# Kernel tuning notes

Measured on AMD Instinct MI355X. Metric: run time of the kernel, lower is better.

The kernel has to match this reference:

```python
import jax, jax.numpy as jnp
import numpy as np

N_NODES = 10000


def _gcn_norm(edge_index, edge_weight, n):
    # PyG GCNConv default: add self-loops (weight 1), symmetric normalization.
    ar = jnp.arange(n, dtype=edge_index.dtype)
    ei = jnp.concatenate([edge_index, jnp.stack([ar, ar])], axis=1)
    ew = jnp.concatenate([edge_weight, jnp.ones((n,), edge_weight.dtype)], axis=0)
    row, col = ei[0], ei[1]
    deg = jax.ops.segment_sum(ew, col, num_segments=n)
    dis = jnp.where(deg > 0, jax.lax.rsqrt(jnp.where(deg > 0, deg, 1.0)), 0.0)
    norm = dis[row] * ew * dis[col]
    return row, col, norm


def _gcn_conv(h, W, b, row, col, norm, n):
    hw = h @ W                                    # [N, out]
    msg = norm[:, None] * hw[row]                 # gather + edge scale
    return jax.ops.segment_sum(msg, col, num_segments=n) + b


def setup_inputs() -> dict:
    key = jax.random.key(0)
    ks = jax.random.split(key, 8)
    N, E, D, H1, H2 = N_NODES, 160000, 256, 128, 64
    return {
        "x": jax.random.normal(ks[0], (N, D), jnp.float32),
        "edge_index": jax.random.randint(ks[1], (2, E), 0, N, jnp.int64 if jax.config.jax_enable_x64 else jnp.int32),
        "edge_weight": jax.random.uniform(ks[2], (E,), jnp.float32),
        "noise": jax.random.normal(ks[3], (N, H2), jnp.float32),
        "W1": jax.random.normal(ks[4], (D, H1), jnp.float32) * (1.0 / np.sqrt(D)),
        "b1": jnp.zeros((H1,), jnp.float32),
        "W2": jax.random.normal(ks[5], (H1, H2), jnp.float32) * (1.0 / np.sqrt(H1)),
        "b2": jnp.zeros((H2,), jnp.float32),
        "W3": jax.random.normal(ks[6], (H1, H2), jnp.float32) * (1.0 / np.sqrt(H1)),
        "b3": jnp.zeros((H2,), jnp.float32),
    }


def reference(x, edge_index, edge_weight, noise, W1, b1, W2, b2, W3, b3):
    n = x.shape[0]
    row, col, norm = _gcn_norm(edge_index, edge_weight, n)
    h = jax.nn.relu(_gcn_conv(x, W1, b1, row, col, norm, n))
    mean = _gcn_conv(h, W2, b2, row, col, norm, n)
    log_std = _gcn_conv(h, W3, b3, row, col, norm, n)
    z = mean + noise * jnp.exp(log_std)           # reparameterization
    adj_rec = jax.nn.sigmoid(z @ z.T)             # [N, N] dot-product decode
    return adj_rec
```

## Files before the change

### kernel.cpp

```cpp
#include <hip/hip_runtime.h>


#define Nn 10000
#define Np 10112
#define NpK (Np * 64)

typedef short short8 __attribute__((ext_vector_type(8)));
typedef float f32x4 __attribute__((ext_vector_type(4)));
typedef unsigned short ushort4e __attribute__((ext_vector_type(4)));

static __device__ __forceinline__ float sigmoidf(float v) {
  return __builtin_amdgcn_rcpf(1.0f + __expf(-v));
}
static __device__ __forceinline__ unsigned short f32_to_bf16(float f) {
  unsigned int u = __float_as_uint(f);
  unsigned int r = (u + 0x7FFF + ((u >> 16) & 1)) >> 16;
  return (unsigned short)r;
}
static __device__ __forceinline__ float bf16_to_f32(unsigned short s) {
  return __uint_as_float(((unsigned int)s) << 16);
}

__global__ void k_init(float* __restrict__ deg, int* __restrict__ cnt, int n,
                       unsigned short* __restrict__ zh, unsigned short* __restrict__ zl) {
  int i = blockIdx.x * 256 + threadIdx.x;
  if (i < n) { deg[i] = 1.0f; cnt[i] = 0; }
  if (i < (Np - Nn) * 64) { zh[Nn * 64 + i] = 0; zl[Nn * 64 + i] = 0; }
}

__global__ void k_edge_pre(const int* __restrict__ col, const float* __restrict__ ew,
                           float* __restrict__ deg, int* __restrict__ cnt, int E) {
  int e = blockIdx.x * 256 + threadIdx.x;
  if (e < E) { int c = col[e]; atomicAdd(&deg[c], ew[e]); atomicAdd(&cnt[c], 1); }
}

__global__ void k_dis(float* __restrict__ deg, int n) {
  int i = blockIdx.x * 256 + threadIdx.x;
  if (i < n) { float d = deg[i]; deg[i] = (d > 0.0f) ? rsqrtf(d) : 0.0f; }
}

__global__ __launch_bounds__(256) void k_scan(const int* __restrict__ cnt,
                                              int* __restrict__ ofs, int* __restrict__ ofs2,
                                              int n) {
  __shared__ int partial[256];
  const int t = threadIdx.x;
  const int CH = (n + 255) / 256;
  const int start = t * CH;
  int local = 0;
  for (int j = 0; j < CH; ++j) {
    int idx = start + j;
    if (idx < n) local += cnt[idx];
  }
  partial[t] = local;
  __syncthreads();
  for (int off = 1; off < 256; off <<= 1) {
    int x = (t >= off) ? partial[t - off] : 0;
    __syncthreads();
    partial[t] += x;
    __syncthreads();
  }
  int run = partial[t] - local;
  for (int j = 0; j < CH; ++j) {
    int idx = start + j;
    if (idx < n) {
      ofs[idx] = run; ofs2[idx] = run;
      run += cnt[idx];
    }
  }
  if (t == 255) { ofs[n] = run; ofs2[n] = run; }
}

__global__ void k_fill(const int* __restrict__ row, const int* __restrict__ col,
                       const float* __restrict__ ew, const float* __restrict__ dis,
                       int* __restrict__ ofs2, int* __restrict__ csr_src,
                       float* __restrict__ csr_w, int E) {
  int e = blockIdx.x * 256 + threadIdx.x;
  if (e < E) {
    int r = row[e], c = col[e];
    int p = atomicAdd(&ofs2[c], 1);
    csr_src[p] = r;
    csr_w[p] = dis[r] * ew[e] * dis[c];
  }
}

__global__ __launch_bounds__(256) void k_gemm1(const float* __restrict__ x,
                                               const float* __restrict__ W1,
                                               float* __restrict__ hw1) {
  __shared__ float xs[16][68];
  __shared__ float ws[64][128];
  const int tid = threadIdx.x;
  const int row0 = blockIdx.x * 16;
  const int j0 = (tid & 31) * 4;
  const int r0 = (tid >> 5) * 2;
  const int lr = tid >> 4, lk = tid & 15;
  float acc0[4] = {0, 0, 0, 0}, acc1[4] = {0, 0, 0, 0};
  for (int k0 = 0; k0 < 256; k0 += 64) {
    *(float4*)&xs[lr][lk * 4] = *(const float4*)&x[(row0 + lr) * 256 + k0 + lk * 4];
#pragma unroll
    for (int it = 0; it < 8; ++it) {
      int idx4 = tid + it * 256;
      int kk = idx4 >> 5, jq = idx4 & 31;
      *(float4*)&ws[kk][jq * 4] = *(const float4*)&W1[(k0 + kk) * 128 + jq * 4];
    }
    __syncthreads();
#pragma unroll 8
    for (int kk = 0; kk < 64; ++kk) {
      float a0 = xs[r0][kk], a1 = xs[r0 + 1][kk];
      float4 w = *(const float4*)&ws[kk][j0];
      acc0[0] += a0 * w.x; acc0[1] += a0 * w.y; acc0[2] += a0 * w.z; acc0[3] += a0 * w.w;
      acc1[0] += a1 * w.x; acc1[1] += a1 * w.y; acc1[2] += a1 * w.z; acc1[3] += a1 * w.w;
    }
    __syncthreads();
  }
  *(float4*)&hw1[(row0 + r0) * 128 + j0] = make_float4(acc0[0], acc0[1], acc0[2], acc0[3]);
  *(float4*)&hw1[(row0 + r0 + 1) * 128 + j0] = make_float4(acc1[0], acc1[1], acc1[2], acc1[3]);
}

__global__ __launch_bounds__(256) void k_agg(const int* __restrict__ ofs,
                                             const int* __restrict__ csr_src,
                                             const float* __restrict__ csr_w,
                                             const float* __restrict__ feat,
                                             const float* __restrict__ dis,
                                             const float* __restrict__ b,
                                             float* __restrict__ out, int n, int mode) {
  int node = blockIdx.x * 4 + (threadIdx.x >> 6);
  if (node >= n) return;
  int f2 = threadIdx.x & 63;
  const float2* featv = (const float2*)feat;
  int s = ofs[node], e = ofs[node + 1];
  float d = dis[node];
  float2 self = featv[node * 64 + f2];
  float accx = d * d * self.x, accy = d * d * self.y;
  int j = s;
  for (; j + 2 <= e; j += 2) {
    int r0 = csr_src[j], r1 = csr_src[j + 1];
    float w0 = csr_w[j], w1 = csr_w[j + 1];
    float2 v0 = featv[r0 * 64 + f2];
    float2 v1 = featv[r1 * 64 + f2];
    accx += w0 * v0.x + w1 * v1.x;
    accy += w0 * v0.y + w1 * v1.y;
  }
  if (j < e) {
    int r0 = csr_src[j];
    float w0 = csr_w[j];
    float2 v0 = featv[r0 * 64 + f2];
    accx += w0 * v0.x;
    accy += w0 * v0.y;
  }
  float2 o;
  if (mode == 0) {
    float2 bb = ((const float2*)b)[f2];
    o.x = fmaxf(accx + bb.x, 0.0f);
    o.y = fmaxf(accy + bb.y, 0.0f);
  } else {
    o.x = accx; o.y = accy;
  }
  ((float2*)out)[node * 64 + f2] = o;
}

__global__ __launch_bounds__(256) void k_gemm2z(const float* __restrict__ hagg,
                                                const float* __restrict__ W2, const float* __restrict__ W3,
                                                const float* __restrict__ b2, const float* __restrict__ b3,
                                                const float* __restrict__ noise,
                                                unsigned short* __restrict__ zh,
                                                unsigned short* __restrict__ zl) {
  __shared__ float xs[16][68];
  __shared__ float ws[64][128];
  __shared__ float zs[16][128];
  const int tid = threadIdx.x;
  const int row0 = blockIdx.x * 16;
  const int j0 = (tid & 31) * 4;
  const int r0 = (tid >> 5) * 2;
  const int lr = tid >> 4, lk = tid & 15;
  float acc0[4] = {0, 0, 0, 0}, acc1[4] = {0, 0, 0, 0};
  for (int k0 = 0; k0 < 128; k0 += 64) {
    *(float4*)&xs[lr][lk * 4] = *(const float4*)&hagg[(row0 + lr) * 128 + k0 + lk * 4];
#pragma unroll
    for (int it = 0; it < 8; ++it) {
      int idx4 = tid + it * 256;
      int kk = idx4 >> 5, jq = idx4 & 31;
      int j = jq * 4;
      float4 wv;
      if (j < 64) wv = *(const float4*)&W2[(k0 + kk) * 64 + j];
      else        wv = *(const float4*)&W3[(k0 + kk) * 64 + (j - 64)];
      *(float4*)&ws[kk][j] = wv;
    }
    __syncthreads();
#pragma unroll 8
    for (int kk = 0; kk < 64; ++kk) {
      float a0 = xs[r0][kk], a1 = xs[r0 + 1][kk];
      float4 w = *(const float4*)&ws[kk][j0];
      acc0[0] += a0 * w.x; acc0[1] += a0 * w.y; acc0[2] += a0 * w.z; acc0[3] += a0 * w.w;
      acc1[0] += a1 * w.x; acc1[1] += a1 * w.y; acc1[2] += a1 * w.z; acc1[3] += a1 * w.w;
    }
    __syncthreads();
  }
  {
    float4 bb = (j0 < 64) ? *(const float4*)&b2[j0] : *(const float4*)&b3[j0 - 64];
    zs[r0][j0 + 0] = acc0[0] + bb.x; zs[r0][j0 + 1] = acc0[1] + bb.y;
    zs[r0][j0 + 2] = acc0[2] + bb.z; zs[r0][j0 + 3] = acc0[3] + bb.w;
    zs[r0 + 1][j0 + 0] = acc1[0] + bb.x; zs[r0 + 1][j0 + 1] = acc1[1] + bb.y;
    zs[r0 + 1][j0 + 2] = acc1[2] + bb.z; zs[r0 + 1][j0 + 3] = acc1[3] + bb.w;
  }
  __syncthreads();
  {
    const int r = tid >> 4;
    const int jj = (tid & 15) * 4;
    float4 mn = *(const float4*)&zs[r][jj];
    float4 ls = *(const float4*)&zs[r][64 + jj];
    float4 nz = *(const float4*)&noise[(row0 + r) * 64 + jj];
    float z0 = mn.x + nz.x * __expf(ls.x);
    float z1 = mn.y + nz.y * __expf(ls.y);
    float z2 = mn.z + nz.z * __expf(ls.z);
    float z3 = mn.w + nz.w * __expf(ls.w);
    ushort4e h, l;
    h[0] = f32_to_bf16(z0); l[0] = f32_to_bf16(z0 - bf16_to_f32(h[0]));
    h[1] = f32_to_bf16(z1); l[1] = f32_to_bf16(z1 - bf16_to_f32(h[1]));
    h[2] = f32_to_bf16(z2); l[2] = f32_to_bf16(z2 - bf16_to_f32(h[2]));
    h[3] = f32_to_bf16(z3); l[3] = f32_to_bf16(z3 - bf16_to_f32(h[3]));
    *(ushort4e*)&zh[(row0 + r) * 64 + jj] = h;
    *(ushort4e*)&zl[(row0 + r) * 64 + jj] = l;
  }
}

__global__ __launch_bounds__(256) void k_decode(const unsigned short* __restrict__ zh,
                                                const unsigned short* __restrict__ zl,
                                                float* __restrict__ out, int n) {
  __shared__ short zhr[128][64];
  __shared__ short zlr[128][64];
  __shared__ short zhc[128][64];
  __shared__ short zlc[128][64];
  const int tid = threadIdx.x;
  const int R0 = blockIdx.y * 128;
  const int C0 = blockIdx.x * 128;

  {
    const int seg = tid & 7;
#pragma unroll
    for (int p = 0; p < 4; ++p) {
      const int rr = (p << 5) + (tid >> 3);
      const int sw = (seg ^ (rr & 7)) * 8;
      short8 vhr = *(const short8*)&zh[(size_t)(R0 + rr) * 64 + seg * 8];
      short8 vlr = *(const short8*)&zl[(size_t)(R0 + rr) * 64 + seg * 8];
      short8 vhc = *(const short8*)&zh[(size_t)(C0 + rr) * 64 + seg * 8];
      short8 vlc = *(const short8*)&zl[(size_t)(C0 + rr) * 64 + seg * 8];
      *(short8*)&zhr[rr][sw] = vhr;
      *(short8*)&zlr[rr][sw] = vlr;
      *(short8*)&zhc[rr][sw] = vhc;
      *(short8*)&zlc[rr][sw] = vlc;
    }
  }
  __syncthreads();

  const int wave = tid >> 6, lane = tid & 63;
  const int lr0 = (wave >> 1) * 64;
  const int lc0 = (wave & 1) * 64;
  const int lrow = lane & 15;
  const int quad = lane >> 4;
  f32x4 acc[4][4];
#pragma unroll
  for (int m = 0; m < 4; ++m)
#pragma unroll
    for (int nn = 0; nn < 4; ++nn) acc[m][nn] = (f32x4){0.0f, 0.0f, 0.0f, 0.0f};

#pragma unroll
  for (int kc = 0; kc < 64; kc += 32) {
    const int cb = (kc >> 3) + quad;
    short8 rh[4], rl[4], ch[4], cl[4];
#pragma unroll
    for (int m = 0; m < 4; ++m) {
      int row = lr0 + m * 16 + lrow;
      int sw = (cb ^ (row & 7)) * 8;
      rh[m] = *(const short8*)&zhr[row][sw];
      rl[m] = *(const short8*)&zlr[row][sw];
    }
#pragma unroll
    for (int nn = 0; nn < 4; ++nn) {
      int row = lc0 + nn * 16 + lrow;
      int sw = (cb ^ (row & 7)) * 8;
      ch[nn] = *(const short8*)&zhc[row][sw];
      cl[nn] = *(const short8*)&zlc[row][sw];
    }
#pragma unroll
    for (int m = 0; m < 4; ++m)
#pragma unroll
      for (int nn = 0; nn < 4; ++nn) {
        acc[m][nn] = __builtin_amdgcn_mfma_f32_16x16x32_bf16(ch[nn], rh[m], acc[m][nn], 0, 0, 0);
        acc[m][nn] = __builtin_amdgcn_mfma_f32_16x16x32_bf16(cl[nn], rh[m], acc[m][nn], 0, 0, 0);
        acc[m][nn] = __builtin_amdgcn_mfma_f32_16x16x32_bf16(ch[nn], rl[m], acc[m][nn], 0, 0, 0);
      }
  }

#pragma unroll
  for (int m = 0; m < 4; ++m) {
    int gr = R0 + lr0 + m * 16 + lrow;
    if (gr >= n) continue;
#pragma unroll
    for (int nn = 0; nn < 4; ++nn) {
      int c0 = C0 + lc0 + nn * 16 + quad * 4;
      if (c0 >= n) continue;
      f32x4 v;
      v[0] = sigmoidf(acc[m][nn][0]);
      v[1] = sigmoidf(acc[m][nn][1]);
      v[2] = sigmoidf(acc[m][nn][2]);
      v[3] = sigmoidf(acc[m][nn][3]);
      *(f32x4*)&out[(size_t)gr * n + c0] = v;
    }
  }
}

extern "C" void kernel_launch(void* const* d_in, const int* in_sizes, int n_in,
                              void* d_out, int out_size, void* d_ws, size_t ws_size,
                              hipStream_t stream) {
  const float* x     = (const float*)d_in[0];
  const int*   ei    = (const int*)d_in[1];
  const float* ew    = (const float*)d_in[2];
  const float* noise = (const float*)d_in[3];
  const float* W1    = (const float*)d_in[4];
  const float* b1    = (const float*)d_in[5];
  const float* W2    = (const float*)d_in[6];
  const float* b2    = (const float*)d_in[7];
  const float* W3    = (const float*)d_in[8];
  const float* b3    = (const float*)d_in[9];
  const int E = in_sizes[2];
  const int n = Nn;
  const int* row = ei;
  const int* col = ei + E;

  float* dis = (float*)d_ws;
  unsigned short* zh = (unsigned short*)((char*)d_ws + 10240 * 4);
  unsigned short* zl = zh + NpK;

  float* S    = (float*)d_out;
  float* hw1  = S;
  float* h    = S + 1310720;
  float* hagg = S + 2621440;
  float* csr_w  = S + 5242880;
  int* csr_src  = (int*)(S + 5402880);
  int* ofs      = (int*)(S + 5562880);
  int* ofs2     = (int*)(S + 5572896);
  int* cnt      = (int*)(S + 5582912);

  k_init<<<(n + 255) / 256, 256, 0, stream>>>(dis, cnt, n, zh, zl);
  k_edge_pre<<<(E + 255) / 256, 256, 0, stream>>>(col, ew, dis, cnt, E);
  k_dis<<<(n + 255) / 256, 256, 0, stream>>>(dis, n);
  k_scan<<<1, 256, 0, stream>>>(cnt, ofs, ofs2, n);
  k_fill<<<(E + 255) / 256, 256, 0, stream>>>(row, col, ew, dis, ofs2, csr_src, csr_w, E);

  k_gemm1<<<n / 16, 256, 0, stream>>>(x, W1, hw1);
  k_agg<<<(n + 3) / 4, 256, 0, stream>>>(ofs, csr_src, csr_w, hw1, dis, b1, h, n, 0);
  k_agg<<<(n + 3) / 4, 256, 0, stream>>>(ofs, csr_src, csr_w, h, dis, b1, hagg, n, 1);

  k_gemm2z<<<n / 16, 256, 0, stream>>>(hagg, W2, W3, b2, b3, noise, zh, zl);

  dim3 g((n + 127) / 128, (n + 127) / 128);
  k_decode<<<g, 256, 0, stream>>>(zh, zl, (float*)d_out, n);
}
```

Measured before the change: 575.4 us.

## Fuse all GCN-VAE stages into one persistent kernel with grid barriers

```diff
diff --git a/kernel.cpp b/kernel.cpp
--- a/kernel.cpp
+++ b/kernel.cpp
@@ -4,10 +4,19 @@
 #define Nn 10000
 #define Np 10112
 #define NpK (Np * 64)
+#define NBLK 448
+#define NTHR (NBLK * 256)
+#define NTILE (79 * 79)
 
 typedef short short8 __attribute__((ext_vector_type(8)));
 typedef float f32x4 __attribute__((ext_vector_type(4)));
 typedef unsigned short ushort4e __attribute__((ext_vector_type(4)));
+
+union SmemT {
+  struct { short zhr[128][64]; short zlr[128][64]; short zhc[128][64]; short zlc[128][64]; } d;
+  struct { float xs[16][68]; float ws[64][128]; float zs[16][128]; } g;
+  int partial[256];
+};
 
 static __device__ __forceinline__ float sigmoidf(float v) {
   return __builtin_amdgcn_rcpf(1.0f + __expf(-v));
@@ -21,290 +30,317 @@
   return __uint_as_float(((unsigned int)s) << 16);
 }
 
-__global__ void k_init(float* __restrict__ deg, int* __restrict__ cnt, int n,
-                       unsigned short* __restrict__ zh, unsigned short* __restrict__ zl) {
-  int i = blockIdx.x * 256 + threadIdx.x;
-  if (i < n) { deg[i] = 1.0f; cnt[i] = 0; }
-  if (i < (Np - Nn) * 64) { zh[Nn * 64 + i] = 0; zl[Nn * 64 + i] = 0; }
-}
-
-__global__ void k_edge_pre(const int* __restrict__ col, const float* __restrict__ ew,
-                           float* __restrict__ deg, int* __restrict__ cnt, int E) {
-  int e = blockIdx.x * 256 + threadIdx.x;
-  if (e < E) { int c = col[e]; atomicAdd(&deg[c], ew[e]); atomicAdd(&cnt[c], 1); }
-}
-
-__global__ void k_dis(float* __restrict__ deg, int n) {
-  int i = blockIdx.x * 256 + threadIdx.x;
-  if (i < n) { float d = deg[i]; deg[i] = (d > 0.0f) ? rsqrtf(d) : 0.0f; }
-}
-
-__global__ __launch_bounds__(256) void k_scan(const int* __restrict__ cnt,
-                                              int* __restrict__ ofs, int* __restrict__ ofs2,
-                                              int n) {
-  __shared__ int partial[256];
-  const int t = threadIdx.x;
-  const int CH = (n + 255) / 256;
-  const int start = t * CH;
-  int local = 0;
-  for (int j = 0; j < CH; ++j) {
-    int idx = start + j;
-    if (idx < n) local += cnt[idx];
-  }
-  partial[t] = local;
+static __device__ __forceinline__ void gsync(unsigned* bar, int slot) {
   __syncthreads();
-  for (int off = 1; off < 256; off <<= 1) {
-    int x = (t >= off) ? partial[t - off] : 0;
-    __syncthreads();
-    partial[t] += x;
-    __syncthreads();
-  }
-  int run = partial[t] - local;
-  for (int j = 0; j < CH; ++j) {
-    int idx = start + j;
-    if (idx < n) {
-      ofs[idx] = run; ofs2[idx] = run;
-      run += cnt[idx];
-    }
-  }
-  if (t == 255) { ofs[n] = run; ofs2[n] = run; }
-}
-
-__global__ void k_fill(const int* __restrict__ row, const int* __restrict__ col,
-                       const float* __restrict__ ew, const float* __restrict__ dis,
-                       int* __restrict__ ofs2, int* __restrict__ csr_src,
-                       float* __restrict__ csr_w, int E) {
-  int e = blockIdx.x * 256 + threadIdx.x;
-  if (e < E) {
-    int r = row[e], c = col[e];
+  if (threadIdx.x == 0) {
+    __hip_atomic_fetch_add(&bar[slot], 1u, __ATOMIC_RELEASE, __HIP_MEMORY_SCOPE_AGENT);
+    while (__hip_atomic_load(&bar[slot], __ATOMIC_RELAXED, __HIP_MEMORY_SCOPE_AGENT) < (unsigned)NBLK)
+      __builtin_amdgcn_s_sleep(2);
+    __threadfence();
+  }
+  __syncthreads();
+}
+
+__global__ void k_barzero(unsigned* __restrict__ bar) {
+  if (threadIdx.x < 16) bar[threadIdx.x] = 0;
+}
+
+__global__ __launch_bounds__(256, 2) void k_mega(
+    const float* __restrict__ x, const int* __restrict__ erow, const int* __restrict__ ecol,
+    const float* __restrict__ ew, const float* __restrict__ noise,
+    const float* __restrict__ W1, const float* __restrict__ b1,
+    const float* __restrict__ W2, const float* __restrict__ b2,
+    const float* __restrict__ W3, const float* __restrict__ b3,
+    float* __restrict__ out, float* __restrict__ dis,
+    unsigned short* __restrict__ zh, unsigned short* __restrict__ zl,
+    unsigned* __restrict__ bar, int E) {
+  __shared__ SmemT sm;
+  const int tid = threadIdx.x;
+  const int bid = blockIdx.x;
+  const int gid = bid * 256 + tid;
+
+  float* S = out;
+  float* hw1  = S;
+  float* h    = S + 1310720;
+  float* hagg = S + 2621440;
+  float* csr_w = S + 5242880;
+  int* csr_src = (int*)(S + 5402880);
+  int* ofs     = (int*)(S + 5562880);
+  int* ofs2    = (int*)(S + 5572896);
+  int* cnt     = (int*)(S + 5582912);
+
+  if (gid < Nn) { dis[gid] = 1.0f; cnt[gid] = 0; }
+  if (gid < (Np - Nn) * 64) { zh[Nn * 64 + gid] = 0; zl[Nn * 64 + gid] = 0; }
+  gsync(bar, 0);
+
+  for (int e = gid; e < E; e += NTHR) {
+    int c = ecol[e];
+    atomicAdd(&dis[c], ew[e]);
+    atomicAdd(&cnt[c], 1);
+  }
+  gsync(bar, 1);
+
+  if (bid == 0) {
+    const int CH = (Nn + 255) / 256;
+    const int start = tid * CH;
+    int local = 0;
+    for (int j = 0; j < CH; ++j) {
+      int idx = start + j;
+      if (idx < Nn) local += cnt[idx];
+    }
+    sm.partial[tid] = local;
+    __syncthreads();
+    for (int off = 1; off < 256; off <<= 1) {
+      int v = (tid >= off) ? sm.partial[tid - off] : 0;
+      __syncthreads();
+      sm.partial[tid] += v;
+      __syncthreads();
+    }
+    int run = sm.partial[tid] - local;
+    for (int j = 0; j < CH; ++j) {
+      int idx = start + j;
+      if (idx < Nn) { ofs[idx] = run; ofs2[idx] = run; run += cnt[idx]; }
+    }
+    if (tid == 255) { ofs[Nn] = run; ofs2[Nn] = run; }
+  } else {
+    int i = (bid - 1) * 256 + tid;
+    if (i < Nn) { float dv = dis[i]; dis[i] = (dv > 0.0f) ? rsqrtf(dv) : 0.0f; }
+  }
+  gsync(bar, 2);
+
+  for (int e = gid; e < E; e += NTHR) {
+    int r = erow[e], c = ecol[e];
     int p = atomicAdd(&ofs2[c], 1);
     csr_src[p] = r;
     csr_w[p] = dis[r] * ew[e] * dis[c];
   }
-}
-
-__global__ __launch_bounds__(256) void k_gemm1(const float* __restrict__ x,
-                                               const float* __restrict__ W1,
-                                               float* __restrict__ hw1) {
-  __shared__ float xs[16][68];
-  __shared__ float ws[64][128];
-  const int tid = threadIdx.x;
-  const int row0 = blockIdx.x * 16;
-  const int j0 = (tid & 31) * 4;
-  const int r0 = (tid >> 5) * 2;
-  const int lr = tid >> 4, lk = tid & 15;
-  float acc0[4] = {0, 0, 0, 0}, acc1[4] = {0, 0, 0, 0};
-  for (int k0 = 0; k0 < 256; k0 += 64) {
-    *(float4*)&xs[lr][lk * 4] = *(const float4*)&x[(row0 + lr) * 256 + k0 + lk * 4];
-#pragma unroll
-    for (int it = 0; it < 8; ++it) {
-      int idx4 = tid + it * 256;
-      int kk = idx4 >> 5, jq = idx4 & 31;
-      *(float4*)&ws[kk][jq * 4] = *(const float4*)&W1[(k0 + kk) * 128 + jq * 4];
-    }
-    __syncthreads();
+  gsync(bar, 3);
+
+  for (int rb = bid; rb < 625; rb += NBLK) {
+    const int row0 = rb * 16;
+    const int j0 = (tid & 31) * 4;
+    const int r0 = (tid >> 5) * 2;
+    const int lr = tid >> 4, lk = tid & 15;
+    float acc0[4] = {0, 0, 0, 0}, acc1[4] = {0, 0, 0, 0};
+    for (int k0 = 0; k0 < 256; k0 += 64) {
+      *(float4*)&sm.g.xs[lr][lk * 4] = *(const float4*)&x[(row0 + lr) * 256 + k0 + lk * 4];
+#pragma unroll
+      for (int it = 0; it < 8; ++it) {
+        int idx4 = tid + it * 256;
+        int kk = idx4 >> 5, jq = idx4 & 31;
+        *(float4*)&sm.g.ws[kk][jq * 4] = *(const float4*)&W1[(k0 + kk) * 128 + jq * 4];
+      }
+      __syncthreads();
 #pragma unroll 8
-    for (int kk = 0; kk < 64; ++kk) {
-      float a0 = xs[r0][kk], a1 = xs[r0 + 1][kk];
-      float4 w = *(const float4*)&ws[kk][j0];
-      acc0[0] += a0 * w.x; acc0[1] += a0 * w.y; acc0[2] += a0 * w.z; acc0[3] += a0 * w.w;
-      acc1[0] += a1 * w.x; acc1[1] += a1 * w.y; acc1[2] += a1 * w.z; acc1[3] += a1 * w.w;
-    }
-    __syncthreads();
-  }
-  *(float4*)&hw1[(row0 + r0) * 128 + j0] = make_float4(acc0[0], acc0[1], acc0[2], acc0[3]);
-  *(float4*)&hw1[(row0 + r0 + 1) * 128 + j0] = make_float4(acc1[0], acc1[1], acc1[2], acc1[3]);
-}
-
-__global__ __launch_bounds__(256) void k_agg(const int* __restrict__ ofs,
-                                             const int* __restrict__ csr_src,
-                                             const float* __restrict__ csr_w,
-                                             const float* __restrict__ feat,
-                                             const float* __restrict__ dis,
-                                             const float* __restrict__ b,
-                                             float* __restrict__ out, int n, int mode) {
-  int node = blockIdx.x * 4 + (threadIdx.x >> 6);
-  if (node >= n) return;
-  int f2 = threadIdx.x & 63;
-  const float2* featv = (const float2*)feat;
-  int s = ofs[node], e = ofs[node + 1];
-  float d = dis[node];
-  float2 self = featv[node * 64 + f2];
-  float accx = d * d * self.x, accy = d * d * self.y;
-  int j = s;
-  for (; j + 2 <= e; j += 2) {
-    int r0 = csr_src[j], r1 = csr_src[j + 1];
-    float w0 = csr_w[j], w1 = csr_w[j + 1];
-    float2 v0 = featv[r0 * 64 + f2];
-    float2 v1 = featv[r1 * 64 + f2];
-    accx += w0 * v0.x + w1 * v1.x;
-    accy += w0 * v0.y + w1 * v1.y;
-  }
-  if (j < e) {
-    int r0 = csr_src[j];
-    float w0 = csr_w[j];
-    float2 v0 = featv[r0 * 64 + f2];
-    accx += w0 * v0.x;
-    accy += w0 * v0.y;
-  }
-  float2 o;
-  if (mode == 0) {
-    float2 bb = ((const float2*)b)[f2];
-    o.x = fmaxf(accx + bb.x, 0.0f);
-    o.y = fmaxf(accy + bb.y, 0.0f);
-  } else {
-    o.x = accx; o.y = accy;
-  }
-  ((float2*)out)[node * 64 + f2] = o;
-}
-
-__global__ __launch_bounds__(256) void k_gemm2z(const float* __restrict__ hagg,
-                                                const float* __restrict__ W2, const float* __restrict__ W3,
-                                                const float* __restrict__ b2, const float* __restrict__ b3,
-                                                const float* __restrict__ noise,
-                                                unsigned short* __restrict__ zh,
-                                                unsigned short* __restrict__ zl) {
-  __shared__ float xs[16][68];
-  __shared__ float ws[64][128];
-  __shared__ float zs[16][128];
-  const int tid = threadIdx.x;
-  const int row0 = blockIdx.x * 16;
-  const int j0 = (tid & 31) * 4;
-  const int r0 = (tid >> 5) * 2;
-  const int lr = tid >> 4, lk = tid & 15;
-  float acc0[4] = {0, 0, 0, 0}, acc1[4] = {0, 0, 0, 0};
-  for (int k0 = 0; k0 < 128; k0 += 64) {
-    *(float4*)&xs[lr][lk * 4] = *(const float4*)&hagg[(row0 + lr) * 128 + k0 + lk * 4];
-#pragma unroll
-    for (int it = 0; it < 8; ++it) {
-      int idx4 = tid + it * 256;
-      int kk = idx4 >> 5, jq = idx4 & 31;
-      int j = jq * 4;
-      float4 wv;
-      if (j < 64) wv = *(const float4*)&W2[(k0 + kk) * 64 + j];
-      else        wv = *(const float4*)&W3[(k0 + kk) * 64 + (j - 64)];
-      *(float4*)&ws[kk][j] = wv;
-    }
-    __syncthreads();
+      for (int kk = 0; kk < 64; ++kk) {
+        float a0 = sm.g.xs[r0][kk], a1 = sm.g.xs[r0 + 1][kk];
+        float4 w = *(const float4*)&sm.g.ws[kk][j0];
+        acc0[0] += a0 * w.x; acc0[1] += a0 * w.y; acc0[2] += a0 * w.z; acc0[3] += a0 * w.w;
+        acc1[0] += a1 * w.x; acc1[1] += a1 * w.y; acc1[2] += a1 * w.z; acc1[3] += a1 * w.w;
+      }
+      __syncthreads();
+    }
+    *(float4*)&hw1[(row0 + r0) * 128 + j0] = make_float4(acc0[0], acc0[1], acc0[2], acc0[3]);
+    *(float4*)&hw1[(row0 + r0 + 1) * 128 + j0] = make_float4(acc1[0], acc1[1], acc1[2], acc1[3]);
+  }
+  gsync(bar, 4);
+
+  {
+    const int f2 = tid & 63;
+    const float2* featv = (const float2*)hw1;
+    for (int node = bid * 4 + (tid >> 6); node < Nn; node += NBLK * 4) {
+      int s = ofs[node], e = ofs[node + 1];
+      float d = dis[node];
+      float2 self = featv[node * 64 + f2];
+      float accx = d * d * self.x, accy = d * d * self.y;
+      int j = s;
+      for (; j + 2 <= e; j += 2) {
+        int r0 = csr_src[j], r1 = csr_src[j + 1];
+        float w0 = csr_w[j], w1 = csr_w[j + 1];
+        float2 v0 = featv[r0 * 64 + f2];
+        float2 v1 = featv[r1 * 64 + f2];
+        accx += w0 * v0.x + w1 * v1.x;
+        accy += w0 * v0.y + w1 * v1.y;
+      }
+      if (j < e) {
+        int r0 = csr_src[j];
+        float w0 = csr_w[j];
+        float2 v0 = featv[r0 * 64 + f2];
+        accx += w0 * v0.x;
+        accy += w0 * v0.y;
+      }
+      float2 bb = ((const float2*)b1)[f2];
+      float2 o;
+      o.x = fmaxf(accx + bb.x, 0.0f);
+      o.y = fmaxf(accy + bb.y, 0.0f);
+      ((float2*)h)[node * 64 + f2] = o;
+    }
+  }
+  gsync(bar, 5);
+  {
+    const int f2 = tid & 63;
+    const float2* featv = (const float2*)h;
+    for (int node = bid * 4 + (tid >> 6); node < Nn; node += NBLK * 4) {
+      int s = ofs[node], e = ofs[node + 1];
+      float d = dis[node];
+      float2 self = featv[node * 64 + f2];
+      float accx = d * d * self.x, accy = d * d * self.y;
+      int j = s;
+      for (; j + 2 <= e; j += 2) {
+        int r0 = csr_src[j], r1 = csr_src[j + 1];
+        float w0 = csr_w[j], w1 = csr_w[j + 1];
+        float2 v0 = featv[r0 * 64 + f2];
+        float2 v1 = featv[r1 * 64 + f2];
+        accx += w0 * v0.x + w1 * v1.x;
+        accy += w0 * v0.y + w1 * v1.y;
+      }
+      if (j < e) {
+        int r0 = csr_src[j];
+        float w0 = csr_w[j];
+        float2 v0 = featv[r0 * 64 + f2];
+        accx += w0 * v0.x;
+        accy += w0 * v0.y;
+      }
+      float2 o; o.x = accx; o.y = accy;
+      ((float2*)hagg)[node * 64 + f2] = o;
+    }
+  }
+  gsync(bar, 6);
+
+  for (int rb = bid; rb < 625; rb += NBLK) {
+    const int row0 = rb * 16;
+    const int j0 = (tid & 31) * 4;
+    const int r0 = (tid >> 5) * 2;
+    const int lr = tid >> 4, lk = tid & 15;
+    float acc0[4] = {0, 0, 0, 0}, acc1[4] = {0, 0, 0, 0};
+    for (int k0 = 0; k0 < 128; k0 += 64) {
+      *(float4*)&sm.g.xs[lr][lk * 4] = *(const float4*)&hagg[(row0 + lr) * 128 + k0 + lk * 4];
+#pragma unroll
+      for (int it = 0; it < 8; ++it) {
+        int idx4 = tid + it * 256;
+        int kk = idx4 >> 5, jq = idx4 & 31;
+        int j = jq * 4;
+        float4 wv;
+        if (j < 64) wv = *(const float4*)&W2[(k0 + kk) * 64 + j];
+        else        wv = *(const float4*)&W3[(k0 + kk) * 64 + (j - 64)];
+        *(float4*)&sm.g.ws[kk][j] = wv;
+      }
+      __syncthreads();
 #pragma unroll 8
-    for (int kk = 0; kk < 64; ++kk) {
-      float a0 = xs[r0][kk], a1 = xs[r0 + 1][kk];
-      float4 w = *(const float4*)&ws[kk][j0];
-      acc0[0] += a0 * w.x; acc0[1] += a0 * w.y; acc0[2] += a0 * w.z; acc0[3] += a0 * w.w;
-      acc1[0] += a1 * w.x; acc1[1] += a1 * w.y; acc1[2] += a1 * w.z; acc1[3] += a1 * w.w;
-    }
-    __syncthreads();
-  }
-  {
-    float4 bb = (j0 < 64) ? *(const float4*)&b2[j0] : *(const float4*)&b3[j0 - 64];
-    zs[r0][j0 + 0] = acc0[0] + bb.x; zs[r0][j0 + 1] = acc0[1] + bb.y;
-    zs[r0][j0 + 2] = acc0[2] + bb.z; zs[r0][j0 + 3] = acc0[3] + bb.w;
-    zs[r0 + 1][j0 + 0] = acc1[0] + bb.x; zs[r0 + 1][j0 + 1] = acc1[1] + bb.y;
-    zs[r0 + 1][j0 + 2] = acc1[2] + bb.z; zs[r0 + 1][j0 + 3] = acc1[3] + bb.w;
-  }
-  __syncthreads();
-  {
-    const int r = tid >> 4;
-    const int jj = (tid & 15) * 4;
-    float4 mn = *(const float4*)&zs[r][jj];
-    float4 ls = *(const float4*)&zs[r][64 + jj];
-    float4 nz = *(const float4*)&noise[(row0 + r) * 64 + jj];
-    float z0 = mn.x + nz.x * __expf(ls.x);
-    float z1 = mn.y + nz.y * __expf(ls.y);
-    float z2 = mn.z + nz.z * __expf(ls.z);
-    float z3 = mn.w + nz.w * __expf(ls.w);
-    ushort4e h, l;
-    h[0] = f32_to_bf16(z0); l[0] = f32_to_bf16(z0 - bf16_to_f32(h[0]));
-    h[1] = f32_to_bf16(z1); l[1] = f32_to_bf16(z1 - bf16_to_f32(h[1]));
-    h[2] = f32_to_bf16(z2); l[2] = f32_to_bf16(z2 - bf16_to_f32(h[2]));
-    h[3] = f32_to_bf16(z3); l[3] = f32_to_bf16(z3 - bf16_to_f32(h[3]));
-    *(ushort4e*)&zh[(row0 + r) * 64 + jj] = h;
-    *(ushort4e*)&zl[(row0 + r) * 64 + jj] = l;
-  }
-}
-
-__global__ __launch_bounds__(256) void k_decode(const unsigned short* __restrict__ zh,
-                                                const unsigned short* __restrict__ zl,
-                                                float* __restrict__ out, int n) {
-  __shared__ short zhr[128][64];
-  __shared__ short zlr[128][64];
-  __shared__ short zhc[128][64];
-  __shared__ short zlc[128][64];
-  const int tid = threadIdx.x;
-  const int R0 = blockIdx.y * 128;
-  const int C0 = blockIdx.x * 128;
-
-  {
-    const int seg = tid & 7;
-#pragma unroll
-    for (int p = 0; p < 4; ++p) {
-      const int rr = (p << 5) + (tid >> 3);
-      const int sw = (seg ^ (rr & 7)) * 8;
-      short8 vhr = *(const short8*)&zh[(size_t)(R0 + rr) * 64 + seg * 8];
-      short8 vlr = *(const short8*)&zl[(size_t)(R0 + rr) * 64 + seg * 8];
-      short8 vhc = *(const short8*)&zh[(size_t)(C0 + rr) * 64 + seg * 8];
-      short8 vlc = *(const short8*)&zl[(size_t)(C0 + rr) * 64 + seg * 8];
-      *(short8*)&zhr[rr][sw] = vhr;
-      *(short8*)&zlr[rr][sw] = vlr;
-      *(short8*)&zhc[rr][sw] = vhc;
-      *(short8*)&zlc[rr][sw] = vlc;
-    }
-  }
-  __syncthreads();
+      for (int kk = 0; kk < 64; ++kk) {
+        float a0 = sm.g.xs[r0][kk], a1 = sm.g.xs[r0 + 1][kk];
+        float4 w = *(const float4*)&sm.g.ws[kk][j0];
+        acc0[0] += a0 * w.x; acc0[1] += a0 * w.y; acc0[2] += a0 * w.z; acc0[3] += a0 * w.w;
+        acc1[0] += a1 * w.x; acc1[1] += a1 * w.y; acc1[2] += a1 * w.z; acc1[3] += a1 * w.w;
+      }
+      __syncthreads();
+    }
+    {
+      float4 bb = (j0 < 64) ? *(const float4*)&b2[j0] : *(const float4*)&b3[j0 - 64];
+      sm.g.zs[r0][j0 + 0] = acc0[0] + bb.x; sm.g.zs[r0][j0 + 1] = acc0[1] + bb.y;
+      sm.g.zs[r0][j0 + 2] = acc0[2] + bb.z; sm.g.zs[r0][j0 + 3] = acc0[3] + bb.w;
+      sm.g.zs[r0 + 1][j0 + 0] = acc1[0] + bb.x; sm.g.zs[r0 + 1][j0 + 1] = acc1[1] + bb.y;
+      sm.g.zs[r0 + 1][j0 + 2] = acc1[2] + bb.z; sm.g.zs[r0 + 1][j0 + 3] = acc1[3] + bb.w;
+    }
+    __syncthreads();
+    {
+      const int r = tid >> 4;
+      const int jj = (tid & 15) * 4;
+      float4 mn = *(const float4*)&sm.g.zs[r][jj];
+      float4 ls = *(const float4*)&sm.g.zs[r][64 + jj];
+      float4 nz = *(const float4*)&noise[(row0 + r) * 64 + jj];
+      float z0 = mn.x + nz.x * __expf(ls.x);
+      float z1 = mn.y + nz.y * __expf(ls.y);
+      float z2 = mn.z + nz.z * __expf(ls.z);
+      float z3 = mn.w + nz.w * __expf(ls.w);
+      ushort4e hh, ll;
+      hh[0] = f32_to_bf16(z0); ll[0] = f32_to_bf16(z0 - bf16_to_f32(hh[0]));
+      hh[1] = f32_to_bf16(z1); ll[1] = f32_to_bf16(z1 - bf16_to_f32(hh[1]));
+      hh[2] = f32_to_bf16(z2); ll[2] = f32_to_bf16(z2 - bf16_to_f32(hh[2]));
+      hh[3] = f32_to_bf16(z3); ll[3] = f32_to_bf16(z3 - bf16_to_f32(hh[3]));
+      *(ushort4e*)&zh[(row0 + r) * 64 + jj] = hh;
+      *(ushort4e*)&zl[(row0 + r) * 64 + jj] = ll;
+    }
+    __syncthreads();
+  }
+  gsync(bar, 7);
 
   const int wave = tid >> 6, lane = tid & 63;
   const int lr0 = (wave >> 1) * 64;
   const int lc0 = (wave & 1) * 64;
   const int lrow = lane & 15;
   const int quad = lane >> 4;
-  f32x4 acc[4][4];
-#pragma unroll
-  for (int m = 0; m < 4; ++m)
-#pragma unroll
-    for (int nn = 0; nn < 4; ++nn) acc[m][nn] = (f32x4){0.0f, 0.0f, 0.0f, 0.0f};
-
-#pragma unroll
-  for (int kc = 0; kc < 64; kc += 32) {
-    const int cb = (kc >> 3) + quad;
-    short8 rh[4], rl[4], ch[4], cl[4];
+  for (int t = bid; t < NTILE; t += NBLK) {
+    const int R0 = (t / 79) * 128;
+    const int C0 = (t % 79) * 128;
+    __syncthreads();
+    {
+      const int seg = tid & 7;
+#pragma unroll
+      for (int p = 0; p < 4; ++p) {
+        const int rr = (p << 5) + (tid >> 3);
+        const int sw = (seg ^ (rr & 7)) * 8;
+        short8 vhr = *(const short8*)&zh[(size_t)(R0 + rr) * 64 + seg * 8];
+        short8 vlr = *(const short8*)&zl[(size_t)(R0 + rr) * 64 + seg * 8];
+        short8 vhc = *(const short8*)&zh[(size_t)(C0 + rr) * 64 + seg * 8];
+        short8 vlc = *(const short8*)&zl[(size_t)(C0 + rr) * 64 + seg * 8];
+        *(short8*)&sm.d.zhr[rr][sw] = vhr;
+        *(short8*)&sm.d.zlr[rr][sw] = vlr;
+        *(short8*)&sm.d.zhc[rr][sw] = vhc;
+        *(short8*)&sm.d.zlc[rr][sw] = vlc;
+      }
+    }
+    __syncthreads();
+
+    f32x4 acc[4][4];
+#pragma unroll
+    for (int m = 0; m < 4; ++m)
+#pragma unroll
+      for (int nn = 0; nn < 4; ++nn) acc[m][nn] = (f32x4){0.0f, 0.0f, 0.0f, 0.0f};
+
+#pragma unroll
+    for (int kc = 0; kc < 64; kc += 32) {
+      const int cb = (kc >> 3) + quad;
+      short8 rh[4], rl[4], ch[4], cl[4];
+#pragma unroll
+      for (int m = 0; m < 4; ++m) {
+        int row = lr0 + m * 16 + lrow;
+        int sw = (cb ^ (row & 7)) * 8;
+        rh[m] = *(const short8*)&sm.d.zhr[row][sw];
+        rl[m] = *(const short8*)&sm.d.zlr[row][sw];
+      }
+#pragma unroll
+      for (int nn = 0; nn < 4; ++nn) {
+        int row = lc0 + nn * 16 + lrow;
+        int sw = (cb ^ (row & 7)) * 8;
+        ch[nn] = *(const short8*)&sm.d.zhc[row][sw];
+        cl[nn] = *(const short8*)&sm.d.zlc[row][sw];
+      }
+#pragma unroll
+      for (int m = 0; m < 4; ++m)
+#pragma unroll
+        for (int nn = 0; nn < 4; ++nn) {
+          acc[m][nn] = __builtin_amdgcn_mfma_f32_16x16x32_bf16(ch[nn], rh[m], acc[m][nn], 0, 0, 0);
+          acc[m][nn] = __builtin_amdgcn_mfma_f32_16x16x32_bf16(cl[nn], rh[m], acc[m][nn], 0, 0, 0);
+          acc[m][nn] = __builtin_amdgcn_mfma_f32_16x16x32_bf16(ch[nn], rl[m], acc[m][nn], 0, 0, 0);
+        }
+    }
+
 #pragma unroll
     for (int m = 0; m < 4; ++m) {
-      int row = lr0 + m * 16 + lrow;
-      int sw = (cb ^ (row & 7)) * 8;
-      rh[m] = *(const short8*)&zhr[row][sw];
-      rl[m] = *(const short8*)&zlr[row][sw];
-    }
-#pragma unroll
-    for (int nn = 0; nn < 4; ++nn) {
-      int row = lc0 + nn * 16 + lrow;
-      int sw = (cb ^ (row & 7)) * 8;
-      ch[nn] = *(const short8*)&zhc[row][sw];
-      cl[nn] = *(const short8*)&zlc[row][sw];
-    }
-#pragma unroll
-    for (int m = 0; m < 4; ++m)
+      int gr = R0 + lr0 + m * 16 + lrow;
+      if (gr >= Nn) continue;
 #pragma unroll
       for (int nn = 0; nn < 4; ++nn) {
-        acc[m][nn] = __builtin_amdgcn_mfma_f32_16x16x32_bf16(ch[nn], rh[m], acc[m][nn], 0, 0, 0);
-        acc[m][nn] = __builtin_amdgcn_mfma_f32_16x16x32_bf16(cl[nn], rh[m], acc[m][nn], 0, 0, 0);
-        acc[m][nn] = __builtin_amdgcn_mfma_f32_16x16x32_bf16(ch[nn], rl[m], acc[m][nn], 0, 0, 0);
-      }
-  }
-
-#pragma unroll
-  for (int m = 0; m < 4; ++m) {
-    int gr = R0 + lr0 + m * 16 + lrow;
-    if (gr >= n) continue;
-#pragma unroll
-    for (int nn = 0; nn < 4; ++nn) {
-      int c0 = C0 + lc0 + nn * 16 + quad * 4;
-      if (c0 >= n) continue;
-      f32x4 v;
-      v[0] = sigmoidf(acc[m][nn][0]);
-      v[1] = sigmoidf(acc[m][nn][1]);
-      v[2] = sigmoidf(acc[m][nn][2]);
-      v[3] = sigmoidf(acc[m][nn][3]);
-      *(f32x4*)&out[(size_t)gr * n + c0] = v;
+        int c0 = C0 + lc0 + nn * 16 + quad * 4;
+        if (c0 >= Nn) continue;
+        f32x4 v;
+        v[0] = sigmoidf(acc[m][nn][0]);
+        v[1] = sigmoidf(acc[m][nn][1]);
+        v[2] = sigmoidf(acc[m][nn][2]);
+        v[3] = sigmoidf(acc[m][nn][3]);
+        *(f32x4*)&out[(size_t)gr * Nn + c0] = v;
+      }
     }
   }
 }
@@ -323,36 +359,15 @@
   const float* W3    = (const float*)d_in[8];
   const float* b3    = (const float*)d_in[9];
   const int E = in_sizes[2];
-  const int n = Nn;
   const int* row = ei;
   const int* col = ei + E;
 
   float* dis = (float*)d_ws;
   unsigned short* zh = (unsigned short*)((char*)d_ws + 10240 * 4);
   unsigned short* zl = zh + NpK;
-
-  float* S    = (float*)d_out;
-  float* hw1  = S;
-  float* h    = S + 1310720;
-  float* hagg = S + 2621440;
-  float* csr_w  = S + 5242880;
-  int* csr_src  = (int*)(S + 5402880);
-  int* ofs      = (int*)(S + 5562880);
-  int* ofs2     = (int*)(S + 5572896);
-  int* cnt      = (int*)(S + 5582912);
-
-  k_init<<<(n + 255) / 256, 256, 0, stream>>>(dis, cnt, n, zh, zl);
-  k_edge_pre<<<(E + 255) / 256, 256, 0, stream>>>(col, ew, dis, cnt, E);
-  k_dis<<<(n + 255) / 256, 256, 0, stream>>>(dis, n);
-  k_scan<<<1, 256, 0, stream>>>(cnt, ofs, ofs2, n);
-  k_fill<<<(E + 255) / 256, 256, 0, stream>>>(row, col, ew, dis, ofs2, csr_src, csr_w, E);
-
-  k_gemm1<<<n / 16, 256, 0, stream>>>(x, W1, hw1);
-  k_agg<<<(n + 3) / 4, 256, 0, stream>>>(ofs, csr_src, csr_w, hw1, dis, b1, h, n, 0);
-  k_agg<<<(n + 3) / 4, 256, 0, stream>>>(ofs, csr_src, csr_w, h, dis, b1, hagg, n, 1);
-
-  k_gemm2z<<<n / 16, 256, 0, stream>>>(hagg, W2, W3, b2, b3, noise, zh, zl);
-
-  dim3 g((n + 127) / 128, (n + 127) / 128);
-  k_decode<<<g, 256, 0, stream>>>(zh, zl, (float*)d_out, n);
-}
+  unsigned* bar = (unsigned*)((char*)d_ws + 10240 * 4 + (size_t)2 * NpK * 2);
+
+  k_barzero<<<1, 64, 0, stream>>>(bar);
+  k_mega<<<NBLK, 256, 0, stream>>>(x, row, col, ew, noise, W1, b1, W2, b2, W3, b3,
+                                   (float*)d_out, dis, zh, zl, bar, E);
+}
```

Result: slower. 957.9 us (+66.5%).

## Fuse graph preprocessing launches and merge second aggregation into GEMM2

Applied to the files above, without the earlier changes.

```diff
diff --git a/kernel.cpp b/kernel.cpp
--- a/kernel.cpp
+++ b/kernel.cpp
@@ -21,53 +21,92 @@
   return __uint_as_float(((unsigned int)s) << 16);
 }
 
-__global__ void k_init(float* __restrict__ deg, int* __restrict__ cnt, int n,
-                       unsigned short* __restrict__ zh, unsigned short* __restrict__ zl) {
-  int i = blockIdx.x * 256 + threadIdx.x;
-  if (i < n) { deg[i] = 1.0f; cnt[i] = 0; }
-  if (i < (Np - Nn) * 64) { zh[Nn * 64 + i] = 0; zl[Nn * 64 + i] = 0; }
-}
-
-__global__ void k_edge_pre(const int* __restrict__ col, const float* __restrict__ ew,
-                           float* __restrict__ deg, int* __restrict__ cnt, int E) {
-  int e = blockIdx.x * 256 + threadIdx.x;
-  if (e < E) { int c = col[e]; atomicAdd(&deg[c], ew[e]); atomicAdd(&cnt[c], 1); }
-}
-
-__global__ void k_dis(float* __restrict__ deg, int n) {
-  int i = blockIdx.x * 256 + threadIdx.x;
-  if (i < n) { float d = deg[i]; deg[i] = (d > 0.0f) ? rsqrtf(d) : 0.0f; }
-}
-
-__global__ __launch_bounds__(256) void k_scan(const int* __restrict__ cnt,
-                                              int* __restrict__ ofs, int* __restrict__ ofs2,
-                                              int n) {
-  __shared__ int partial[256];
-  const int t = threadIdx.x;
-  const int CH = (n + 255) / 256;
-  const int start = t * CH;
-  int local = 0;
-  for (int j = 0; j < CH; ++j) {
-    int idx = start + j;
-    if (idx < n) local += cnt[idx];
-  }
-  partial[t] = local;
-  __syncthreads();
-  for (int off = 1; off < 256; off <<= 1) {
-    int x = (t >= off) ? partial[t - off] : 0;
-    __syncthreads();
-    partial[t] += x;
-    __syncthreads();
-  }
-  int run = partial[t] - local;
-  for (int j = 0; j < CH; ++j) {
-    int idx = start + j;
-    if (idx < n) {
-      ofs[idx] = run; ofs2[idx] = run;
-      run += cnt[idx];
-    }
-  }
-  if (t == 255) { ofs[n] = run; ofs2[n] = run; }
+__global__ __launch_bounds__(256) void k_front(const float* __restrict__ x,
+                                               const float* __restrict__ W1,
+                                               float* __restrict__ hw1,
+                                               const int* __restrict__ ecol,
+                                               const float* __restrict__ ew,
+                                               float* __restrict__ deg,
+                                               int* __restrict__ cnt, int E) {
+  const int tid = threadIdx.x;
+  const int bid = blockIdx.x;
+  if (bid >= 625) {
+    for (int e = (bid - 625) * 256 + tid; e < E; e += 157 * 256) {
+      int c = ecol[e];
+      atomicAdd(&deg[c], ew[e]);
+      atomicAdd(&cnt[c], 1);
+    }
+    return;
+  }
+  __shared__ float xs[16][68];
+  __shared__ float ws[64][128];
+  const int row0 = bid * 16;
+  const int j0 = (tid & 31) * 4;
+  const int r0 = (tid >> 5) * 2;
+  const int lr = tid >> 4, lk = tid & 15;
+  float acc0[4] = {0, 0, 0, 0}, acc1[4] = {0, 0, 0, 0};
+  for (int k0 = 0; k0 < 256; k0 += 64) {
+    *(float4*)&xs[lr][lk * 4] = *(const float4*)&x[(row0 + lr) * 256 + k0 + lk * 4];
+#pragma unroll
+    for (int it = 0; it < 8; ++it) {
+      int idx4 = tid + it * 256;
+      int kk = idx4 >> 5, jq = idx4 & 31;
+      *(float4*)&ws[kk][jq * 4] = *(const float4*)&W1[(k0 + kk) * 128 + jq * 4];
+    }
+    __syncthreads();
+#pragma unroll 8
+    for (int kk = 0; kk < 64; ++kk) {
+      float a0 = xs[r0][kk], a1 = xs[r0 + 1][kk];
+      float4 w = *(const float4*)&ws[kk][j0];
+      acc0[0] += a0 * w.x; acc0[1] += a0 * w.y; acc0[2] += a0 * w.z; acc0[3] += a0 * w.w;
+      acc1[0] += a1 * w.x; acc1[1] += a1 * w.y; acc1[2] += a1 * w.z; acc1[3] += a1 * w.w;
+    }
+    __syncthreads();
+  }
+  *(float4*)&hw1[(row0 + r0) * 128 + j0] = make_float4(acc0[0], acc0[1], acc0[2], acc0[3]);
+  *(float4*)&hw1[(row0 + r0 + 1) * 128 + j0] = make_float4(acc1[0], acc1[1], acc1[2], acc1[3]);
+}
+
+__global__ __launch_bounds__(256) void k_mid(const int* __restrict__ cnt,
+                                             int* __restrict__ ofs, int* __restrict__ ofs2,
+                                             float* __restrict__ deg,
+                                             unsigned short* __restrict__ zh,
+                                             unsigned short* __restrict__ zl) {
+  const int tid = threadIdx.x;
+  const int bid = blockIdx.x;
+  if (bid == 0) {
+    __shared__ int partial[256];
+    const int CH = (Nn + 255) / 256;
+    const int start = tid * CH;
+    int local = 0;
+    for (int j = 0; j < CH; ++j) {
+      int idx = start + j;
+      if (idx < Nn) local += cnt[idx];
+    }
+    partial[tid] = local;
+    __syncthreads();
+    for (int off = 1; off < 256; off <<= 1) {
+      int v = (tid >= off) ? partial[tid - off] : 0;
+      __syncthreads();
+      partial[tid] += v;
+      __syncthreads();
+    }
+    int run = partial[tid] - local;
+    for (int j = 0; j < CH; ++j) {
+      int idx = start + j;
+      if (idx < Nn) { ofs[idx] = run; ofs2[idx] = run; run += cnt[idx]; }
+    }
+    if (tid == 255) { ofs[Nn] = run; ofs2[Nn] = run; }
+  } else if (bid <= 40) {
+    int i = (bid - 1) * 256 + tid;
+    if (i < Nn) deg[i] = rsqrtf(deg[i] + 1.0f);
+  } else {
+    int local = (bid - 41) * 256 + tid;
+    if (local < (Np - Nn) * 64 / 4) {
+      ((ushort4e*)(zh + Nn * 64))[local] = (ushort4e){0, 0, 0, 0};
+      ((ushort4e*)(zl + Nn * 64))[local] = (ushort4e){0, 0, 0, 0};
+    }
+  }
 }
 
 __global__ void k_fill(const int* __restrict__ row, const int* __restrict__ col,
@@ -83,46 +122,13 @@
   }
 }
 
-__global__ __launch_bounds__(256) void k_gemm1(const float* __restrict__ x,
-                                               const float* __restrict__ W1,
-                                               float* __restrict__ hw1) {
-  __shared__ float xs[16][68];
-  __shared__ float ws[64][128];
-  const int tid = threadIdx.x;
-  const int row0 = blockIdx.x * 16;
-  const int j0 = (tid & 31) * 4;
-  const int r0 = (tid >> 5) * 2;
-  const int lr = tid >> 4, lk = tid & 15;
-  float acc0[4] = {0, 0, 0, 0}, acc1[4] = {0, 0, 0, 0};
-  for (int k0 = 0; k0 < 256; k0 += 64) {
-    *(float4*)&xs[lr][lk * 4] = *(const float4*)&x[(row0 + lr) * 256 + k0 + lk * 4];
-#pragma unroll
-    for (int it = 0; it < 8; ++it) {
-      int idx4 = tid + it * 256;
-      int kk = idx4 >> 5, jq = idx4 & 31;
-      *(float4*)&ws[kk][jq * 4] = *(const float4*)&W1[(k0 + kk) * 128 + jq * 4];
-    }
-    __syncthreads();
-#pragma unroll 8
-    for (int kk = 0; kk < 64; ++kk) {
-      float a0 = xs[r0][kk], a1 = xs[r0 + 1][kk];
-      float4 w = *(const float4*)&ws[kk][j0];
-      acc0[0] += a0 * w.x; acc0[1] += a0 * w.y; acc0[2] += a0 * w.z; acc0[3] += a0 * w.w;
-      acc1[0] += a1 * w.x; acc1[1] += a1 * w.y; acc1[2] += a1 * w.z; acc1[3] += a1 * w.w;
-    }
-    __syncthreads();
-  }
-  *(float4*)&hw1[(row0 + r0) * 128 + j0] = make_float4(acc0[0], acc0[1], acc0[2], acc0[3]);
-  *(float4*)&hw1[(row0 + r0 + 1) * 128 + j0] = make_float4(acc1[0], acc1[1], acc1[2], acc1[3]);
-}
-
 __global__ __launch_bounds__(256) void k_agg(const int* __restrict__ ofs,
                                              const int* __restrict__ csr_src,
                                              const float* __restrict__ csr_w,
                                              const float* __restrict__ feat,
                                              const float* __restrict__ dis,
                                              const float* __restrict__ b,
-                                             float* __restrict__ out, int n, int mode) {
+                                             float* __restrict__ out, int n) {
   int node = blockIdx.x * 4 + (threadIdx.x >> 6);
   if (node >= n) return;
   int f2 = threadIdx.x & 63;
@@ -147,34 +153,63 @@
     accx += w0 * v0.x;
     accy += w0 * v0.y;
   }
+  float2 bb = ((const float2*)b)[f2];
   float2 o;
-  if (mode == 0) {
-    float2 bb = ((const float2*)b)[f2];
-    o.x = fmaxf(accx + bb.x, 0.0f);
-    o.y = fmaxf(accy + bb.y, 0.0f);
-  } else {
-    o.x = accx; o.y = accy;
-  }
+  o.x = fmaxf(accx + bb.x, 0.0f);
+  o.y = fmaxf(accy + bb.y, 0.0f);
   ((float2*)out)[node * 64 + f2] = o;
 }
 
-__global__ __launch_bounds__(256) void k_gemm2z(const float* __restrict__ hagg,
+__global__ __launch_bounds__(256) void k_aggemm(const int* __restrict__ ofs,
+                                                const int* __restrict__ csr_src,
+                                                const float* __restrict__ csr_w,
+                                                const float* __restrict__ feat,
+                                                const float* __restrict__ dis,
                                                 const float* __restrict__ W2, const float* __restrict__ W3,
                                                 const float* __restrict__ b2, const float* __restrict__ b3,
                                                 const float* __restrict__ noise,
                                                 unsigned short* __restrict__ zh,
                                                 unsigned short* __restrict__ zl) {
-  __shared__ float xs[16][68];
+  __shared__ float xsf[16][130];
   __shared__ float ws[64][128];
   __shared__ float zs[16][128];
   const int tid = threadIdx.x;
   const int row0 = blockIdx.x * 16;
+  const int w = tid >> 6, f2 = tid & 63;
+  const float2* featv = (const float2*)feat;
+
+#pragma unroll
+  for (int i = 0; i < 4; ++i) {
+    const int nl = w * 4 + i;
+    const int node = row0 + nl;
+    int s = ofs[node], e = ofs[node + 1];
+    float d = dis[node];
+    float2 self = featv[node * 64 + f2];
+    float accx = d * d * self.x, accy = d * d * self.y;
+    int j = s;
+    for (; j + 2 <= e; j += 2) {
+      int r0 = csr_src[j], r1 = csr_src[j + 1];
+      float w0 = csr_w[j], w1 = csr_w[j + 1];
+      float2 v0 = featv[r0 * 64 + f2];
+      float2 v1 = featv[r1 * 64 + f2];
+      accx += w0 * v0.x + w1 * v1.x;
+      accy += w0 * v0.y + w1 * v1.y;
+    }
+    if (j < e) {
+      int r0 = csr_src[j];
+      float w0 = csr_w[j];
+      float2 v0 = featv[r0 * 64 + f2];
+      accx += w0 * v0.x;
+      accy += w0 * v0.y;
+    }
+    *(float2*)&xsf[nl][2 * f2] = make_float2(accx, accy);
+  }
+  __syncthreads();
+
   const int j0 = (tid & 31) * 4;
   const int r0 = (tid >> 5) * 2;
-  const int lr = tid >> 4, lk = tid & 15;
   float acc0[4] = {0, 0, 0, 0}, acc1[4] = {0, 0, 0, 0};
   for (int k0 = 0; k0 < 128; k0 += 64) {
-    *(float4*)&xs[lr][lk * 4] = *(const float4*)&hagg[(row0 + lr) * 128 + k0 + lk * 4];
 #pragma unroll
     for (int it = 0; it < 8; ++it) {
       int idx4 = tid + it * 256;
@@ -188,10 +223,10 @@
     __syncthreads();
 #pragma unroll 8
     for (int kk = 0; kk < 64; ++kk) {
-      float a0 = xs[r0][kk], a1 = xs[r0 + 1][kk];
-      float4 w = *(const float4*)&ws[kk][j0];
-      acc0[0] += a0 * w.x; acc0[1] += a0 * w.y; acc0[2] += a0 * w.z; acc0[3] += a0 * w.w;
-      acc1[0] += a1 * w.x; acc1[1] += a1 * w.y; acc1[2] += a1 * w.z; acc1[3] += a1 * w.w;
+      float a0 = xsf[r0][k0 + kk], a1 = xsf[r0 + 1][k0 + kk];
+      float4 wv = *(const float4*)&ws[kk][j0];
+      acc0[0] += a0 * wv.x; acc0[1] += a0 * wv.y; acc0[2] += a0 * wv.z; acc0[3] += a0 * wv.w;
+      acc1[0] += a1 * wv.x; acc1[1] += a1 * wv.y; acc1[2] += a1 * wv.z; acc1[3] += a1 * wv.w;
     }
     __syncthreads();
   }
@@ -203,6 +238,7 @@
     zs[r0 + 1][j0 + 2] = acc1[2] + bb.z; zs[r0 + 1][j0 + 3] = acc1[3] + bb.w;
   }
   __syncthreads();
+
   {
     const int r = tid >> 4;
     const int jj = (tid & 15) * 4;
@@ -213,13 +249,13 @@
     float z1 = mn.y + nz.y * __expf(ls.y);
     float z2 = mn.z + nz.z * __expf(ls.z);
     float z3 = mn.w + nz.w * __expf(ls.w);
-    ushort4e h, l;
-    h[0] = f32_to_bf16(z0); l[0] = f32_to_bf16(z0 - bf16_to_f32(h[0]));
-    h[1] = f32_to_bf16(z1); l[1] = f32_to_bf16(z1 - bf16_to_f32(h[1]));
-    h[2] = f32_to_bf16(z2); l[2] = f32_to_bf16(z2 - bf16_to_f32(h[2]));
-    h[3] = f32_to_bf16(z3); l[3] = f32_to_bf16(z3 - bf16_to_f32(h[3]));
-    *(ushort4e*)&zh[(row0 + r) * 64 + jj] = h;
-    *(ushort4e*)&zl[(row0 + r) * 64 + jj] = l;
+    ushort4e hh, ll;
+    hh[0] = f32_to_bf16(z0); ll[0] = f32_to_bf16(z0 - bf16_to_f32(hh[0]));
+    hh[1] = f32_to_bf16(z1); ll[1] = f32_to_bf16(z1 - bf16_to_f32(hh[1]));
+    hh[2] = f32_to_bf16(z2); ll[2] = f32_to_bf16(z2 - bf16_to_f32(hh[2]));
+    hh[3] = f32_to_bf16(z3); ll[3] = f32_to_bf16(z3 - bf16_to_f32(hh[3]));
+    *(ushort4e*)&zh[(row0 + r) * 64 + jj] = hh;
+    *(ushort4e*)&zl[(row0 + r) * 64 + jj] = ll;
   }
 }
 
@@ -328,30 +364,27 @@
   const int* col = ei + E;
 
   float* dis = (float*)d_ws;
-  unsigned short* zh = (unsigned short*)((char*)d_ws + 10240 * 4);
+  int*   cnt = (int*)((char*)d_ws + 10240 * 4);
+  unsigned short* zh = (unsigned short*)((char*)d_ws + 81920);
   unsigned short* zl = zh + NpK;
 
-  float* S    = (float*)d_out;
-  float* hw1  = S;
-  float* h    = S + 1310720;
-  float* hagg = S + 2621440;
-  float* csr_w  = S + 5242880;
-  int* csr_src  = (int*)(S + 5402880);
-  int* ofs      = (int*)(S + 5562880);
-  int* ofs2     = (int*)(S + 5572896);
-  int* cnt      = (int*)(S + 5582912);
-
-  k_init<<<(n + 255) / 256, 256, 0, stream>>>(dis, cnt, n, zh, zl);
-  k_edge_pre<<<(E + 255) / 256, 256, 0, stream>>>(col, ew, dis, cnt, E);
-  k_dis<<<(n + 255) / 256, 256, 0, stream>>>(dis, n);
-  k_scan<<<1, 256, 0, stream>>>(cnt, ofs, ofs2, n);
+  float* S = (float*)d_out;
+  float* hw1   = S;
+  float* h     = S + 1310720;
+  float* csr_w = S + 5242880;
+  int* csr_src = (int*)(S + 5402880);
+  int* ofs     = (int*)(S + 5562880);
+  int* ofs2    = (int*)(S + 5572896);
+
+  hipMemsetAsync(d_ws, 0, 81920, stream);
+
+  k_front<<<782, 256, 0, stream>>>(x, W1, hw1, col, ew, dis, cnt, E);
+  k_mid<<<48, 256, 0, stream>>>(cnt, ofs, ofs2, dis, zh, zl);
   k_fill<<<(E + 255) / 256, 256, 0, stream>>>(row, col, ew, dis, ofs2, csr_src, csr_w, E);
 
-  k_gemm1<<<n / 16, 256, 0, stream>>>(x, W1, hw1);
-  k_agg<<<(n + 3) / 4, 256, 0, stream>>>(ofs, csr_src, csr_w, hw1, dis, b1, h, n, 0);
-  k_agg<<<(n + 3) / 4, 256, 0, stream>>>(ofs, csr_src, csr_w, h, dis, b1, hagg, n, 1);
-
-  k_gemm2z<<<n / 16, 256, 0, stream>>>(hagg, W2, W3, b2, b3, noise, zh, zl);
+  k_agg<<<(n + 3) / 4, 256, 0, stream>>>(ofs, csr_src, csr_w, hw1, dis, b1, h, n);
+  k_aggemm<<<n / 16, 256, 0, stream>>>(ofs, csr_src, csr_w, h, dis, W2, W3, b2, b3,
+                                       noise, zh, zl);
 
   dim3 g((n + 127) / 128, (n + 127) / 128);
   k_decode<<<g, 256, 0, stream>>>(zh, zl, (float*)d_out, n);
```

Result: faster. 559.4 us (-2.8%).
